# Kernel optimization log

Measured on AMD Instinct MI355X. Metric: run time of the kernel, lower is better.

Reference implementation:

```python
import jax, jax.numpy as jnp
import numpy as np
import math

B, L, DM = 8, 4096, 512            # batch, seq len (LQ == LK required by mean-fill quirk), model dim
DK, DV, C = 512, 512, 5            # projected dims, sampling factor
U_K = min(int(C * math.ceil(math.log(L))), L)  # 45 sampled keys
U_Q = min(int(C * math.ceil(math.log(L))), L)  # 45 top queries
SCALE = 1.0 / math.sqrt(DM)        # original divides by sqrt(d) where d = input dm


def setup_inputs() -> dict:
    key = jax.random.key(0)
    ks = jax.random.split(key, 10)
    w = 1.0 / math.sqrt(DM)
    # sample key indices per batch WITHOUT replacement (matches jax.random.choice(replace=False))
    kidx = jax.vmap(lambda k: jax.random.choice(k, L, shape=(U_K,), replace=False))(
        jax.random.split(ks[9], B)).astype(jnp.int32)
    return {
        "Q": jax.random.normal(ks[0], (B, L, DM), jnp.float32),
        "K": jax.random.normal(ks[1], (B, L, DM), jnp.float32),
        "V": jax.random.normal(ks[2], (B, L, DM), jnp.float32),
        "WQ": jax.random.normal(ks[3], (DM, DK), jnp.float32) * w,
        "bQ": jnp.zeros((DK,), jnp.float32),
        "WK": jax.random.normal(ks[4], (DM, DK), jnp.float32) * w,
        "bK": jnp.zeros((DK,), jnp.float32),
        "WV": jax.random.normal(ks[5], (DM, DV), jnp.float32) * w,
        "bV": jnp.zeros((DV,), jnp.float32),
        "kidx": kidx,
    }


def reference(Q, K, V, WQ, bQ, WK, bK, WV, bV, kidx):
    # dense projections (compute-dominant)
    Qp = Q @ WQ + bQ          # [B, L, DK]
    Kp = K @ WK + bK          # [B, L, DK]
    Vp = V @ WV + bV          # [B, L, DV]

    def per_sample(qp, kp, vp, idx):
        kbar = kp[idx]                                 # [U_K, DK] random key gather
        sbar = qp @ kbar.T                             # [L, U_K] sampled scores
        meas = jnp.max(sbar, axis=1) - jnp.mean(sbar, axis=1)  # sparsity measurement [L]
        _, I = jax.lax.top_k(meas, U_Q)                # top-u query indices
        qbar = qp[I]                                   # [U_Q, DK]
        attn = jax.nn.softmax(qbar @ kp.T * SCALE, axis=-1)    # [U_Q, L]
        s1 = attn @ vp                                 # [U_Q, DV]
        # faithful quirk: mean over FEATURE axis of V, broadcast to [L, DV]
        base = jnp.broadcast_to(jnp.mean(vp, axis=1, keepdims=True), (L, DV))
        return base.at[I].set(s1)                      # scatter selected rows

    return jax.vmap(per_sample)(Qp, Kp, Vp, kidx)      # [B, L, DV]
```

## Files before the change

kernel.cpp:

```cpp
#include <hip/hip_runtime.h>
#include <math.h>

static constexpr int B_ = 8;
static constexpr int L_ = 4096;
static constexpr int D_ = 512;
static constexpr int U_ = 45;
static constexpr float SCALE_ = 0.04419417382415922f;

static constexpr size_t OFF_WVMEAN = 0;
static constexpr size_t OFF_BV     = 512;
static constexpr size_t OFF_WQT    = 576;
static constexpr size_t OFF_WKT    = OFF_WQT + 262144;
static constexpr size_t OFF_KBAR   = OFF_WKT + 262144;
static constexpr size_t OFF_KW     = OFF_KBAR + 184320;
static constexpr size_t OFF_CVEC   = OFF_KW + 184320;
static constexpr size_t OFF_MEAS   = OFF_CVEC + 384;
static constexpr size_t OFF_TOPI   = OFF_MEAS + 32768;
static constexpr size_t OFF_QBAR   = OFF_TOPI + 384;
static constexpr size_t OFF_QW     = OFF_QBAR + 184320;
static constexpr size_t OFF_DVEC   = OFF_QW + 184320;
static constexpr size_t OFF_SC     = OFF_DVEC + 384;
static constexpr size_t OFF_PART   = OFF_SC + 1474560;
static constexpr size_t OFF_ATTNV  = OFF_PART + 1474560;
static constexpr size_t OFF_S1     = OFF_ATTNV + 184320;

__device__ __forceinline__ float wave_sum(float v) {
  #pragma unroll
  for (int m = 32; m; m >>= 1) v += __shfl_xor(v, m, 64);
  return v;
}
__device__ __forceinline__ float wave_max(float v) {
  #pragma unroll
  for (int m = 32; m; m >>= 1) v = fmaxf(v, __shfl_xor(v, m, 64));
  return v;
}

__global__ __launch_bounds__(256) void transpose_k(const float* __restrict__ WQ,
    const float* __restrict__ WK, float* __restrict__ wqt, float* __restrict__ wkt) {
  const float* src = blockIdx.z ? WK : WQ;
  float* dst = blockIdx.z ? wkt : wqt;
  __shared__ float tile[32][33];
  int tx = threadIdx.x, ty = threadIdx.y;
  int x = blockIdx.x * 32 + tx;
  int y0 = blockIdx.y * 32;
  for (int r = ty; r < 32; r += 8) tile[r][tx] = src[(size_t)(y0 + r) * 512 + x];
  __syncthreads();
  int xo = y0 + tx;
  int yo0 = blockIdx.x * 32;
  for (int r = ty; r < 32; r += 8) dst[(size_t)(yo0 + r) * 512 + xo] = tile[tx][r];
}

__global__ __launch_bounds__(256) void wvmean_k(const float* __restrict__ WV,
    const float* __restrict__ bV, float* __restrict__ wvmean, float* __restrict__ bvout) {
  int t = threadIdx.x, w = t >> 6, lane = t & 63;
  const float4* W4 = (const float4*)WV;
  int mbase = (blockIdx.x * 4 + w) * 16;
  for (int i = 0; i < 16; ++i) {
    int m = mbase + i;
    float4 a = W4[(size_t)m * 128 + lane];
    float4 c = W4[(size_t)m * 128 + 64 + lane];
    float s = ((a.x + a.y) + (a.z + a.w)) + ((c.x + c.y) + (c.z + c.w));
    s = wave_sum(s);
    if (lane == 0) wvmean[m] = s * (1.0f / 512.0f);
  }
  if (blockIdx.x == 0 && w == 0) {
    const float4* b4 = (const float4*)bV;
    float4 a = b4[lane], c = b4[64 + lane];
    float s = ((a.x + a.y) + (a.z + a.w)) + ((c.x + c.y) + (c.z + c.w));
    s = wave_sum(s);
    if (lane == 0) bvout[0] = s * (1.0f / 512.0f);
  }
}

__global__ __launch_bounds__(512) void rows_matmul_k(const float* __restrict__ src,
    const int* __restrict__ idx, const float* __restrict__ W, const float* __restrict__ bias,
    const float* __restrict__ avec, float* __restrict__ aux, float* __restrict__ out) {
  int blk = blockIdx.x;
  int b = blk / 9, g = blk % 9;
  int j0 = g * 5;
  int t = threadIdx.x;
  __shared__ float rows[5][512];
  for (int r = 0; r < 5; ++r) {
    int j = j0 + r;
    const float* s = idx ? (src + ((size_t)b * L_ + idx[b * U_ + j]) * 512)
                         : (src + ((size_t)(b * U_ + j)) * 512);
    rows[r][t] = s[t];
  }
  __syncthreads();
  float bi = bias ? bias[t] : 0.0f;
  float a0 = bi, a1 = bi, a2 = bi, a3 = bi, a4 = bi;
  #pragma unroll 4
  for (int m = 0; m < 512; ++m) {
    float wv = W[(size_t)m * 512 + t];
    a0 = fmaf(rows[0][m], wv, a0);
    a1 = fmaf(rows[1][m], wv, a1);
    a2 = fmaf(rows[2][m], wv, a2);
    a3 = fmaf(rows[3][m], wv, a3);
    a4 = fmaf(rows[4][m], wv, a4);
  }
  out[((size_t)(b * U_ + j0 + 0)) * 512 + t] = a0;
  out[((size_t)(b * U_ + j0 + 1)) * 512 + t] = a1;
  out[((size_t)(b * U_ + j0 + 2)) * 512 + t] = a2;
  out[((size_t)(b * U_ + j0 + 3)) * 512 + t] = a3;
  out[((size_t)(b * U_ + j0 + 4)) * 512 + t] = a4;
  if (avec) {
    float av = avec[t];
    __shared__ float red[8];
    float accs[5] = {a0, a1, a2, a3, a4};
    #pragma unroll
    for (int r = 0; r < 5; ++r) {
      float v = wave_sum(accs[r] * av);
      if ((t & 63) == 0) red[t >> 6] = v;
      __syncthreads();
      if (t == 0) {
        float s2 = 0.0f;
        #pragma unroll
        for (int k2 = 0; k2 < 8; ++k2) s2 += red[k2];
        aux[b * U_ + j0 + r] = s2;
      }
      __syncthreads();
    }
  }
}

__global__ __launch_bounds__(256) void meas2_k(const float* __restrict__ Q,
    const float* __restrict__ kw, const float* __restrict__ cvec, float* __restrict__ meas) {
  const int b = blockIdx.y;
  const int l0 = blockIdx.x * 64;
  const int t = threadIdx.x;
  const int tx = t & 15, ty = t >> 4;
  const int rswz = (ty >> 1) & 3;

  __shared__ float Qs[64][68];
  __shared__ float Ks[48][68];

  float acc[4][3];
  #pragma unroll
  for (int i = 0; i < 4; ++i) { acc[i][0] = 0.f; acc[i][1] = 0.f; acc[i][2] = 0.f; }

  const float4* Q4  = (const float4*)(Q + ((size_t)b * L_ + l0) * 512);
  const float4* kw4 = (const float4*)(kw + (size_t)b * U_ * 512);

  float4 pq[4], pk[3];
  int lr[4], lc[4], kr[3], kc[3];
  #pragma unroll
  for (int p = 0; p < 4; ++p) { int idx = p * 256 + t; lr[p] = idx >> 4; lc[p] = idx & 15; }
  #pragma unroll
  for (int p = 0; p < 3; ++p) { int idx = p * 256 + t; kr[p] = idx >> 4; kc[p] = idx & 15; }

  #pragma unroll
  for (int p = 0; p < 4; ++p) pq[p] = Q4[(size_t)lr[p] * 128 + lc[p]];
  #pragma unroll
  for (int p = 0; p < 3; ++p)
    pk[p] = (kr[p] < U_) ? kw4[(size_t)kr[p] * 128 + kc[p]] : make_float4(0.f, 0.f, 0.f, 0.f);

  #pragma unroll
  for (int p = 0; p < 4; ++p) {
    int sw = (lr[p] >> 3) & 3;
    *(float4*)&Qs[lr[p]][(lc[p] ^ sw) * 4] = pq[p];
  }
  #pragma unroll
  for (int p = 0; p < 3; ++p) *(float4*)&Ks[kr[p]][kc[p] * 4] = pk[p];
  __syncthreads();

  for (int it = 0; it < 8; ++it) {
    if (it < 7) {
      int k0 = (it + 1) * 16;
      #pragma unroll
      for (int p = 0; p < 4; ++p) pq[p] = Q4[(size_t)lr[p] * 128 + k0 + lc[p]];
      #pragma unroll
      for (int p = 0; p < 3; ++p)
        pk[p] = (kr[p] < U_) ? kw4[(size_t)kr[p] * 128 + k0 + kc[p]] : make_float4(0.f, 0.f, 0.f, 0.f);
    }
    #pragma unroll 4
    for (int kk4 = 0; kk4 < 16; ++kk4) {
      float4 kv0 = *(const float4*)&Ks[tx * 3 + 0][kk4 * 4];
      float4 kv1 = *(const float4*)&Ks[tx * 3 + 1][kk4 * 4];
      float4 kv2 = *(const float4*)&Ks[tx * 3 + 2][kk4 * 4];
      int qc = (kk4 ^ rswz) * 4;
      #pragma unroll
      for (int i = 0; i < 4; ++i) {
        float4 qv = *(const float4*)&Qs[ty * 4 + i][qc];
        acc[i][0] = fmaf(qv.x, kv0.x, acc[i][0]); acc[i][0] = fmaf(qv.y, kv0.y, acc[i][0]);
        acc[i][0] = fmaf(qv.z, kv0.z, acc[i][0]); acc[i][0] = fmaf(qv.w, kv0.w, acc[i][0]);
        acc[i][1] = fmaf(qv.x, kv1.x, acc[i][1]); acc[i][1] = fmaf(qv.y, kv1.y, acc[i][1]);
        acc[i][1] = fmaf(qv.z, kv1.z, acc[i][1]); acc[i][1] = fmaf(qv.w, kv1.w, acc[i][1]);
        acc[i][2] = fmaf(qv.x, kv2.x, acc[i][2]); acc[i][2] = fmaf(qv.y, kv2.y, acc[i][2]);
        acc[i][2] = fmaf(qv.z, kv2.z, acc[i][2]); acc[i][2] = fmaf(qv.w, kv2.w, acc[i][2]);
      }
    }
    __syncthreads();
    if (it < 7) {
      #pragma unroll
      for (int p = 0; p < 4; ++p) {
        int sw = (lr[p] >> 3) & 3;
        *(float4*)&Qs[lr[p]][(lc[p] ^ sw) * 4] = pq[p];
      }
      #pragma unroll
      for (int p = 0; p < 3; ++p) *(float4*)&Ks[kr[p]][kc[p] * 4] = pk[p];
      __syncthreads();
    }
  }

  const bool valid = (tx < 15);
  float c0 = 0.f, c1 = 0.f, c2 = 0.f;
  if (valid) {
    c0 = cvec[b * U_ + tx * 3 + 0];
    c1 = cvec[b * U_ + tx * 3 + 1];
    c2 = cvec[b * U_ + tx * 3 + 2];
  }
  #pragma unroll
  for (int i = 0; i < 4; ++i) {
    float s0 = acc[i][0] + c0, s1 = acc[i][1] + c1, s2 = acc[i][2] + c2;
    float jmax = valid ? fmaxf(fmaxf(s0, s1), s2) : -3.4e38f;
    float jsum = valid ? (s0 + s1 + s2) : 0.f;
    #pragma unroll
    for (int m = 8; m; m >>= 1) {
      jmax = fmaxf(jmax, __shfl_xor(jmax, m, 64));
      jsum += __shfl_xor(jsum, m, 64);
    }
    if (tx == 0) meas[(size_t)b * L_ + l0 + ty * 4 + i] = jmax - jsum * (1.0f / 45.0f);
  }
}

__global__ __launch_bounds__(256) void scores2_k(const float* __restrict__ K,
    const float* __restrict__ qw, const float* __restrict__ dvec, float* __restrict__ sc) {
  const int b = blockIdx.y;
  const int l0 = blockIdx.x * 64;
  const int t = threadIdx.x;
  const int tx = t & 15, ty = t >> 4;
  const int rswz = (ty >> 1) & 3;

  __shared__ float Qs[64][68];
  __shared__ float Ks[48][68];

  float acc[4][3];
  #pragma unroll
  for (int i = 0; i < 4; ++i) { acc[i][0] = 0.f; acc[i][1] = 0.f; acc[i][2] = 0.f; }

  const float4* K4  = (const float4*)(K + ((size_t)b * L_ + l0) * 512);
  const float4* qw4 = (const float4*)(qw + (size_t)b * U_ * 512);

  float4 pq[4], pk[3];
  int lr[4], lc[4], kr[3], kc[3];
  #pragma unroll
  for (int p = 0; p < 4; ++p) { int idx = p * 256 + t; lr[p] = idx >> 4; lc[p] = idx & 15; }
  #pragma unroll
  for (int p = 0; p < 3; ++p) { int idx = p * 256 + t; kr[p] = idx >> 4; kc[p] = idx & 15; }

  #pragma unroll
  for (int p = 0; p < 4; ++p) pq[p] = K4[(size_t)lr[p] * 128 + lc[p]];
  #pragma unroll
  for (int p = 0; p < 3; ++p)
    pk[p] = (kr[p] < U_) ? qw4[(size_t)kr[p] * 128 + kc[p]] : make_float4(0.f, 0.f, 0.f, 0.f);

  #pragma unroll
  for (int p = 0; p < 4; ++p) {
    int sw = (lr[p] >> 3) & 3;
    *(float4*)&Qs[lr[p]][(lc[p] ^ sw) * 4] = pq[p];
  }
  #pragma unroll
  for (int p = 0; p < 3; ++p) *(float4*)&Ks[kr[p]][kc[p] * 4] = pk[p];
  __syncthreads();

  for (int it = 0; it < 8; ++it) {
    if (it < 7) {
      int k0 = (it + 1) * 16;
      #pragma unroll
      for (int p = 0; p < 4; ++p) pq[p] = K4[(size_t)lr[p] * 128 + k0 + lc[p]];
      #pragma unroll
      for (int p = 0; p < 3; ++p)
        pk[p] = (kr[p] < U_) ? qw4[(size_t)kr[p] * 128 + k0 + kc[p]] : make_float4(0.f, 0.f, 0.f, 0.f);
    }
    #pragma unroll 4
    for (int kk4 = 0; kk4 < 16; ++kk4) {
      float4 kv0 = *(const float4*)&Ks[tx * 3 + 0][kk4 * 4];
      float4 kv1 = *(const float4*)&Ks[tx * 3 + 1][kk4 * 4];
      float4 kv2 = *(const float4*)&Ks[tx * 3 + 2][kk4 * 4];
      int qc = (kk4 ^ rswz) * 4;
      #pragma unroll
      for (int i = 0; i < 4; ++i) {
        float4 qv = *(const float4*)&Qs[ty * 4 + i][qc];
        acc[i][0] = fmaf(qv.x, kv0.x, acc[i][0]); acc[i][0] = fmaf(qv.y, kv0.y, acc[i][0]);
        acc[i][0] = fmaf(qv.z, kv0.z, acc[i][0]); acc[i][0] = fmaf(qv.w, kv0.w, acc[i][0]);
        acc[i][1] = fmaf(qv.x, kv1.x, acc[i][1]); acc[i][1] = fmaf(qv.y, kv1.y, acc[i][1]);
        acc[i][1] = fmaf(qv.z, kv1.z, acc[i][1]); acc[i][1] = fmaf(qv.w, kv1.w, acc[i][1]);
        acc[i][2] = fmaf(qv.x, kv2.x, acc[i][2]); acc[i][2] = fmaf(qv.y, kv2.y, acc[i][2]);
        acc[i][2] = fmaf(qv.z, kv2.z, acc[i][2]); acc[i][2] = fmaf(qv.w, kv2.w, acc[i][2]);
      }
    }
    __syncthreads();
    if (it < 7) {
      #pragma unroll
      for (int p = 0; p < 4; ++p) {
        int sw = (lr[p] >> 3) & 3;
        *(float4*)&Qs[lr[p]][(lc[p] ^ sw) * 4] = pq[p];
      }
      #pragma unroll
      for (int p = 0; p < 3; ++p) *(float4*)&Ks[kr[p]][kc[p] * 4] = pk[p];
      __syncthreads();
    }
  }

  if (tx < 15) {
    float d0 = dvec[b * U_ + tx * 3 + 0];
    float d1 = dvec[b * U_ + tx * 3 + 1];
    float d2 = dvec[b * U_ + tx * 3 + 2];
    #pragma unroll
    for (int i = 0; i < 4; ++i) {
      int l = l0 + ty * 4 + i;
      sc[((size_t)(b * U_ + tx * 3 + 0)) * 4096 + l] = (acc[i][0] + d0) * SCALE_;
      sc[((size_t)(b * U_ + tx * 3 + 1)) * 4096 + l] = (acc[i][1] + d1) * SCALE_;
      sc[((size_t)(b * U_ + tx * 3 + 2)) * 4096 + l] = (acc[i][2] + d2) * SCALE_;
    }
  }
}

__global__ __launch_bounds__(256) void topk_k(const float* __restrict__ meas, int* __restrict__ topI) {
  int b = blockIdx.x, t = threadIdx.x;
  __shared__ unsigned long long keys[4096];
  __shared__ unsigned long long wred[4];
  for (int i = t; i < 4096; i += 256) {
    float m = meas[(size_t)b * 4096 + i];
    unsigned u = __float_as_uint(m);
    u = (u & 0x80000000u) ? ~u : (u | 0x80000000u);
    keys[i] = ((unsigned long long)u << 32) | (unsigned)(4095 - i);
  }
  __syncthreads();
  for (int it = 0; it < U_; ++it) {
    unsigned long long lm = 0ull;
    for (int i = t; i < 4096; i += 256) { unsigned long long k = keys[i]; lm = k > lm ? k : lm; }
    #pragma unroll
    for (int m = 32; m; m >>= 1) { unsigned long long o = __shfl_xor(lm, m, 64); lm = o > lm ? o : lm; }
    if ((t & 63) == 0) wred[t >> 6] = lm;
    __syncthreads();
    if (t == 0) {
      unsigned long long f = wred[0];
      for (int k2 = 1; k2 < 4; ++k2) f = wred[k2] > f ? wred[k2] : f;
      int idxl = 4095 - (int)(f & 0xFFFFFFFFull);
      topI[b * U_ + it] = idxl;
      keys[idxl] = 0ull;
    }
    __syncthreads();
  }
}

__global__ __launch_bounds__(256) void softmax_k(float* __restrict__ sc) {
  int row = blockIdx.x;
  int t = threadIdx.x;
  float* s = sc + (size_t)row * 4096;
  __shared__ float buf[4096];
  __shared__ float red[4];
  float4* b4 = (float4*)buf;
  float4* s4 = (float4*)s;
  float lmax = -3.4e38f;
  for (int i = t; i < 1024; i += 256) {
    float4 v = s4[i]; b4[i] = v;
    lmax = fmaxf(lmax, fmaxf(fmaxf(v.x, v.y), fmaxf(v.z, v.w)));
  }
  lmax = wave_max(lmax);
  if ((t & 63) == 0) red[t >> 6] = lmax;
  __syncthreads();
  float mx = fmaxf(fmaxf(red[0], red[1]), fmaxf(red[2], red[3]));
  __syncthreads();
  float lsum = 0.0f;
  for (int i = t; i < 1024; i += 256) {
    float4 v = b4[i];
    v.x = expf(v.x - mx); v.y = expf(v.y - mx); v.z = expf(v.z - mx); v.w = expf(v.w - mx);
    b4[i] = v;
    lsum += (v.x + v.y) + (v.z + v.w);
  }
  lsum = wave_sum(lsum);
  if ((t & 63) == 0) red[t >> 6] = lsum;
  __syncthreads();
  float inv = 1.0f / (red[0] + red[1] + red[2] + red[3]);
  for (int i = t; i < 1024; i += 256) {
    float4 v = b4[i];
    v.x *= inv; v.y *= inv; v.z *= inv; v.w *= inv;
    s4[i] = v;
  }
}

__global__ __launch_bounds__(256) void attnv5_k(const float* __restrict__ V,
    const float* __restrict__ attn, float* __restrict__ part) {
  const int b = blockIdx.x, ks = blockIdx.y, dh = blockIdx.z;
  const int d0 = dh * 64;
  const int t = threadIdx.x;
  const int tx = t & 15, ty = t >> 4;

  __shared__ float As[2][48][68];
  __shared__ float Vs[2][64][68];

  const float* attnb = attn + (size_t)b * U_ * 4096 + (size_t)ks * 512;
  const float* Vb = V + ((size_t)b * L_ + (size_t)ks * 512) * 512 + d0;

  const int vrow = t >> 4, vc4 = t & 15;
  int arow[3], ac4[3], arr[3];
  #pragma unroll
  for (int p = 0; p < 3; ++p) {
    int idx = p * 256 + t;
    arow[p] = idx >> 4; ac4[p] = idx & 15;
    arr[p] = arow[p] < U_ ? arow[p] : U_ - 1;
  }

  float4 pv0, pv1, pv2, pv3, pa0, pa1, pa2;

#define ISSUE(S) do { const int lb_ = (S) * 64;                                  \
    pv0 = *(const float4*)&Vb[(size_t)(lb_ + vrow +  0) * 512 + vc4 * 4];        \
    pv1 = *(const float4*)&Vb[(size_t)(lb_ + vrow + 16) * 512 + vc4 * 4];        \
    pv2 = *(const float4*)&Vb[(size_t)(lb_ + vrow + 32) * 512 + vc4 * 4];        \
    pv3 = *(const float4*)&Vb[(size_t)(lb_ + vrow + 48) * 512 + vc4 * 4];        \
    pa0 = *(const float4*)&attnb[(size_t)arr[0] * 4096 + lb_ + ac4[0] * 4];      \
    pa1 = *(const float4*)&attnb[(size_t)arr[1] * 4096 + lb_ + ac4[1] * 4];      \
    pa2 = *(const float4*)&attnb[(size_t)arr[2] * 4096 + lb_ + ac4[2] * 4];      \
  } while (0)

#define COMMIT(BUF) do {                                                         \
    *(float4*)&Vs[BUF][vrow +  0][vc4 * 4] = pv0;                                \
    *(float4*)&Vs[BUF][vrow + 16][vc4 * 4] = pv1;                                \
    *(float4*)&Vs[BUF][vrow + 32][vc4 * 4] = pv2;                                \
    *(float4*)&Vs[BUF][vrow + 48][vc4 * 4] = pv3;                                \
    *(float4*)&As[BUF][arow[0]][ac4[0] * 4] = pa0;                               \
    *(float4*)&As[BUF][arow[1]][ac4[1] * 4] = pa1;                               \
    *(float4*)&As[BUF][arow[2]][ac4[2] * 4] = pa2;                               \
  } while (0)

  float4 acc0 = make_float4(0.f, 0.f, 0.f, 0.f);
  float4 acc1 = make_float4(0.f, 0.f, 0.f, 0.f);
  float4 acc2 = make_float4(0.f, 0.f, 0.f, 0.f);

  ISSUE(0);
  asm volatile("s_waitcnt vmcnt(0)" ::: "memory");
  COMMIT(0);
  ISSUE(1);
  asm volatile("s_waitcnt lgkmcnt(0)" ::: "memory");
  __builtin_amdgcn_s_barrier();
  __builtin_amdgcn_sched_barrier(0);

  #pragma unroll 1
  for (int s = 0; s < 8; ++s) {
    const int rb = s & 1;
    #pragma unroll 4
    for (int l4 = 0; l4 < 16; ++l4) {
      float4 q0 = *(const float4*)&As[rb][tx * 3 + 0][l4 * 4];
      float4 q1 = *(const float4*)&As[rb][tx * 3 + 1][l4 * 4];
      float4 q2 = *(const float4*)&As[rb][tx * 3 + 2][l4 * 4];
      #pragma unroll
      for (int j = 0; j < 4; ++j) {
        float4 v = *(const float4*)&Vs[rb][l4 * 4 + j][ty * 4];
        float a0 = (j == 0) ? q0.x : (j == 1) ? q0.y : (j == 2) ? q0.z : q0.w;
        float a1 = (j == 0) ? q1.x : (j == 1) ? q1.y : (j == 2) ? q1.z : q1.w;
        float a2 = (j == 0) ? q2.x : (j == 1) ? q2.y : (j == 2) ? q2.z : q2.w;
        acc0.x = fmaf(a0, v.x, acc0.x); acc0.y = fmaf(a0, v.y, acc0.y);
        acc0.z = fmaf(a0, v.z, acc0.z); acc0.w = fmaf(a0, v.w, acc0.w);
        acc1.x = fmaf(a1, v.x, acc1.x); acc1.y = fmaf(a1, v.y, acc1.y);
        acc1.z = fmaf(a1, v.z, acc1.z); acc1.w = fmaf(a1, v.w, acc1.w);
        acc2.x = fmaf(a2, v.x, acc2.x); acc2.y = fmaf(a2, v.y, acc2.y);
        acc2.z = fmaf(a2, v.z, acc2.z); acc2.w = fmaf(a2, v.w, acc2.w);
      }
    }
    if (s + 1 < 8) {
      asm volatile("s_waitcnt vmcnt(0)" ::: "memory");
      COMMIT((s + 1) & 1);
      if (s + 2 < 8) ISSUE(s + 2);
      asm volatile("s_waitcnt lgkmcnt(0)" ::: "memory");
      __builtin_amdgcn_s_barrier();
      __builtin_amdgcn_sched_barrier(0);
    }
  }
#undef ISSUE
#undef COMMIT

  {
    float* dstbase = part + (((size_t)(ks * 8 + b)) * U_) * 512 + d0 + ty * 4;
    int i0 = tx * 3;
    if (i0 + 0 < U_) *(float4*)(dstbase + (size_t)(i0 + 0) * 512) = acc0;
    if (i0 + 1 < U_) *(float4*)(dstbase + (size_t)(i0 + 1) * 512) = acc1;
    if (i0 + 2 < U_) *(float4*)(dstbase + (size_t)(i0 + 2) * 512) = acc2;
  }
}

__global__ __launch_bounds__(256) void attnvred_k(const float* __restrict__ part,
                                                  float* __restrict__ av) {
  int x = blockIdx.x * 256 + threadIdx.x;
  float s = 0.0f;
  #pragma unroll
  for (int ls = 0; ls < 8; ++ls) s += part[(size_t)ls * 184320 + x];
  av[x] = s;
}

__global__ __launch_bounds__(256) void output_k(const float* __restrict__ V,
    const float* __restrict__ wvmean, const float* __restrict__ bvp,
    const int* __restrict__ topI, const float* __restrict__ s1, float* __restrict__ outp) {
  int b = blockIdx.y, tile = blockIdx.x;
  int l0 = tile * 64;
  int t = threadIdx.x, w = t >> 6, lane = t & 63;
  __shared__ int sel[64];
  if (t < 64) sel[t] = -1;
  __syncthreads();
  if (t < U_) {
    int lj = topI[b * U_ + t] - l0;
    if (lj >= 0 && lj < 64) sel[lj] = t;
  }
  __syncthreads();
  const float4* wv4 = (const float4*)wvmean;
  float4 wa = wv4[lane], wb = wv4[64 + lane];
  float bv = bvp[0];
  const float4* V4 = (const float4*)(V + (size_t)b * L_ * 512);
  float4* out4 = (float4*)(outp + (size_t)b * L_ * 512);
  const float4* s14 = (const float4*)s1;
  for (int r = w; r < 64; r += 4) {
    int l = l0 + r;
    int j = sel[r];
    float4 o1, o2;
    if (j >= 0) {
      o1 = s14[((size_t)(b * U_ + j)) * 128 + lane];
      o2 = s14[((size_t)(b * U_ + j)) * 128 + 64 + lane];
    } else {
      float4 va = V4[(size_t)l * 128 + lane];
      float4 vb = V4[(size_t)l * 128 + 64 + lane];
      float s = va.x * wa.x + va.y * wa.y + va.z * wa.z + va.w * wa.w
              + vb.x * wb.x + vb.y * wb.y + vb.z * wb.z + vb.w * wb.w;
      s = wave_sum(s);
      float base = s + bv;
      o1 = make_float4(base, base, base, base);
      o2 = o1;
    }
    out4[(size_t)l * 128 + lane] = o1;
    out4[(size_t)l * 128 + 64 + lane] = o2;
  }
}

extern "C" void kernel_launch(void* const* d_in, const int* in_sizes, int n_in,
                              void* d_out, int out_size, void* d_ws, size_t ws_size,
                              hipStream_t stream) {
  (void)in_sizes; (void)n_in; (void)out_size; (void)ws_size;
  const float* Q  = (const float*)d_in[0];
  const float* K  = (const float*)d_in[1];
  const float* V  = (const float*)d_in[2];
  const float* WQ = (const float*)d_in[3];
  const float* bQ = (const float*)d_in[4];
  const float* WK = (const float*)d_in[5];
  const float* bK = (const float*)d_in[6];
  const float* WV = (const float*)d_in[7];
  const float* bV = (const float*)d_in[8];
  const int* kidx = (const int*)d_in[9];
  float* ws = (float*)d_ws;
  float* out = (float*)d_out;

  float* wvmean = ws + OFF_WVMEAN;
  float* bvm    = ws + OFF_BV;
  float* wqt    = ws + OFF_WQT;
  float* wkt    = ws + OFF_WKT;
  float* kbar   = ws + OFF_KBAR;
  float* kw     = ws + OFF_KW;
  float* cvec   = ws + OFF_CVEC;
  float* measp  = ws + OFF_MEAS;
  int*   topI   = (int*)(ws + OFF_TOPI);
  float* qbar   = ws + OFF_QBAR;
  float* qw     = ws + OFF_QW;
  float* dvec   = ws + OFF_DVEC;
  float* sc     = ws + OFF_SC;
  float* partp  = ws + OFF_PART;
  float* attnv  = ws + OFF_ATTNV;
  float* s1     = ws + OFF_S1;

  transpose_k<<<dim3(16, 16, 2), dim3(32, 8), 0, stream>>>(WQ, WK, wqt, wkt);
  wvmean_k<<<dim3(8), dim3(256), 0, stream>>>(WV, bV, wvmean, bvm);

  rows_matmul_k<<<dim3(72), dim3(512), 0, stream>>>(K, kidx, WK, bK, bQ, cvec, kbar);
  rows_matmul_k<<<dim3(72), dim3(512), 0, stream>>>(kbar, nullptr, wqt, nullptr, nullptr, nullptr, kw);
  meas2_k<<<dim3(64, 8), dim3(256), 0, stream>>>(Q, kw, cvec, measp);
  topk_k<<<dim3(8), dim3(256), 0, stream>>>(measp, topI);
  rows_matmul_k<<<dim3(72), dim3(512), 0, stream>>>(Q, topI, WQ, bQ, bK, dvec, qbar);
  rows_matmul_k<<<dim3(72), dim3(512), 0, stream>>>(qbar, nullptr, wkt, nullptr, nullptr, nullptr, qw);
  scores2_k<<<dim3(64, 8), dim3(256), 0, stream>>>(K, qw, dvec, sc);
  softmax_k<<<dim3(360), dim3(256), 0, stream>>>(sc);
  attnv5_k<<<dim3(8, 8, 8), dim3(256), 0, stream>>>(V, sc, partp);
  attnvred_k<<<dim3(720), dim3(256), 0, stream>>>(partp, attnv);
  rows_matmul_k<<<dim3(72), dim3(512), 0, stream>>>(attnv, nullptr, WV, bV, nullptr, nullptr, s1);
  output_k<<<dim3(64, 8), dim3(256), 0, stream>>>(V, wvmean, bvm, topI, s1, out);
}
```

Baseline: 447.3 us.

## Double-buffer LDS and enlarge tiles in sampled-score GEMM kernels

Replaces the meas2/scores2 kernels with a shared macro-based kernel that tiles 128 rows per block with 6 key columns per thread, and double-buffers the Q/K tiles in LDS. It issues the global loads two stages ahead and uses explicit waitcnt/s_barrier, so each k-step needs one barrier instead of two. Out-of-range key rows are clamped rather than zero-filled, and those columns are masked at the end. The aim is to overlap global loads with FMA work and raise arithmetic intensity per LDS read. The cost is more LDS and registers, and only half as many blocks (256), which may lower occupancy.

```diff
diff --git a/kernel.cpp b/kernel.cpp
--- a/kernel.cpp
+++ b/kernel.cpp
@@ -123,198 +123,145 @@
   }
 }
 
-__global__ __launch_bounds__(256) void meas2_k(const float* __restrict__ Q,
+
+#define M3_DECLS                                                               \
+  const int t = threadIdx.x;                                                   \
+  const int tx = t & 7, ty = t >> 3;                                           \
+  const int qsw = ty & 3;                                                      \
+  __shared__ float Qs[2][128][68];                                             \
+  __shared__ float Ks[2][48][68];                                              \
+  int lr[8], lc[8], kr[3], kc[3], krr[3];                                      \
+  _Pragma("unroll") for (int p = 0; p < 8; ++p) {                              \
+    int idx = p * 256 + t; lr[p] = idx >> 4; lc[p] = idx & 15; }               \
+  _Pragma("unroll") for (int p = 0; p < 3; ++p) {                              \
+    int idx = p * 256 + t; kr[p] = idx >> 4; kc[p] = idx & 15;                 \
+    krr[p] = kr[p] < U_ ? kr[p] : U_ - 1; }                                    \
+  float4 pq[8], pk[3];                                                         \
+  float acc[4][6];                                                             \
+  _Pragma("unroll") for (int i = 0; i < 4; ++i)                                \
+    _Pragma("unroll") for (int r = 0; r < 6; ++r) acc[i][r] = 0.f;
+
+#define M3_ISSUE(S) do { const int k0_ = (S) * 16;                             \
+    _Pragma("unroll") for (int p = 0; p < 8; ++p)                              \
+      pq[p] = X4[(size_t)lr[p] * 128 + k0_ + lc[p]];                           \
+    _Pragma("unroll") for (int p = 0; p < 3; ++p)                              \
+      pk[p] = W4[(size_t)krr[p] * 128 + k0_ + kc[p]];                          \
+  } while (0)
+
+#define M3_COMMIT(B) do {                                                      \
+    _Pragma("unroll") for (int p = 0; p < 8; ++p)                              \
+      *(float4*)&Qs[B][lr[p]][(lc[p] ^ ((lr[p] >> 2) & 3)) * 4] = pq[p];       \
+    _Pragma("unroll") for (int p = 0; p < 3; ++p)                              \
+      *(float4*)&Ks[B][kr[p]][kc[p] * 4] = pk[p];                              \
+  } while (0)
+
+#define M3_PIPELINE                                                            \
+  M3_ISSUE(0);                                                                 \
+  asm volatile("s_waitcnt vmcnt(0)" ::: "memory");                             \
+  M3_COMMIT(0);                                                                \
+  M3_ISSUE(1);                                                                 \
+  asm volatile("s_waitcnt lgkmcnt(0)" ::: "memory");                           \
+  __builtin_amdgcn_s_barrier();                                                \
+  __builtin_amdgcn_sched_barrier(0);                                           \
+  _Pragma("unroll 1")                                                          \
+  for (int s = 0; s < 8; ++s) {                                                \
+    const int rb = s & 1;                                                      \
+    _Pragma("unroll 4")                                                        \
+    for (int kk4 = 0; kk4 < 16; ++kk4) {                                       \
+      float4 kv0 = *(const float4*)&Ks[rb][tx * 6 + 0][kk4 * 4];               \
+      float4 kv1 = *(const float4*)&Ks[rb][tx * 6 + 1][kk4 * 4];               \
+      float4 kv2 = *(const float4*)&Ks[rb][tx * 6 + 2][kk4 * 4];               \
+      float4 kv3 = *(const float4*)&Ks[rb][tx * 6 + 3][kk4 * 4];               \
+      float4 kv4 = *(const float4*)&Ks[rb][tx * 6 + 4][kk4 * 4];               \
+      float4 kv5 = *(const float4*)&Ks[rb][tx * 6 + 5][kk4 * 4];               \
+      const int qc = (kk4 ^ qsw) * 4;                                          \
+      _Pragma("unroll") for (int i = 0; i < 4; ++i) {                          \
+        float4 qv = *(const float4*)&Qs[rb][ty * 4 + i][qc];                   \
+        acc[i][0] = fmaf(qv.x, kv0.x, acc[i][0]); acc[i][0] = fmaf(qv.y, kv0.y, acc[i][0]); \
+        acc[i][0] = fmaf(qv.z, kv0.z, acc[i][0]); acc[i][0] = fmaf(qv.w, kv0.w, acc[i][0]); \
+        acc[i][1] = fmaf(qv.x, kv1.x, acc[i][1]); acc[i][1] = fmaf(qv.y, kv1.y, acc[i][1]); \
+        acc[i][1] = fmaf(qv.z, kv1.z, acc[i][1]); acc[i][1] = fmaf(qv.w, kv1.w, acc[i][1]); \
+        acc[i][2] = fmaf(qv.x, kv2.x, acc[i][2]); acc[i][2] = fmaf(qv.y, kv2.y, acc[i][2]); \
+        acc[i][2] = fmaf(qv.z, kv2.z, acc[i][2]); acc[i][2] = fmaf(qv.w, kv2.w, acc[i][2]); \
+        acc[i][3] = fmaf(qv.x, kv3.x, acc[i][3]); acc[i][3] = fmaf(qv.y, kv3.y, acc[i][3]); \
+        acc[i][3] = fmaf(qv.z, kv3.z, acc[i][3]); acc[i][3] = fmaf(qv.w, kv3.w, acc[i][3]); \
+        acc[i][4] = fmaf(qv.x, kv4.x, acc[i][4]); acc[i][4] = fmaf(qv.y, kv4.y, acc[i][4]); \
+        acc[i][4] = fmaf(qv.z, kv4.z, acc[i][4]); acc[i][4] = fmaf(qv.w, kv4.w, acc[i][4]); \
+        acc[i][5] = fmaf(qv.x, kv5.x, acc[i][5]); acc[i][5] = fmaf(qv.y, kv5.y, acc[i][5]); \
+        acc[i][5] = fmaf(qv.z, kv5.z, acc[i][5]); acc[i][5] = fmaf(qv.w, kv5.w, acc[i][5]); \
+      }                                                                        \
+    }                                                                          \
+    if (s + 1 < 8) {                                                           \
+      asm volatile("s_waitcnt vmcnt(0)" ::: "memory");                         \
+      M3_COMMIT((s + 1) & 1);                                                  \
+      if (s + 2 < 8) M3_ISSUE(s + 2);                                          \
+      asm volatile("s_waitcnt lgkmcnt(0)" ::: "memory");                       \
+      __builtin_amdgcn_s_barrier();                                            \
+      __builtin_amdgcn_sched_barrier(0);                                       \
+    }                                                                          \
+  }
+
+__global__ __launch_bounds__(256) void meas3_k(const float* __restrict__ Q,
     const float* __restrict__ kw, const float* __restrict__ cvec, float* __restrict__ meas) {
   const int b = blockIdx.y;
-  const int l0 = blockIdx.x * 64;
-  const int t = threadIdx.x;
-  const int tx = t & 15, ty = t >> 4;
-  const int rswz = (ty >> 1) & 3;
-
-  __shared__ float Qs[64][68];
-  __shared__ float Ks[48][68];
-
-  float acc[4][3];
-  #pragma unroll
-  for (int i = 0; i < 4; ++i) { acc[i][0] = 0.f; acc[i][1] = 0.f; acc[i][2] = 0.f; }
-
-  const float4* Q4  = (const float4*)(Q + ((size_t)b * L_ + l0) * 512);
-  const float4* kw4 = (const float4*)(kw + (size_t)b * U_ * 512);
-
-  float4 pq[4], pk[3];
-  int lr[4], lc[4], kr[3], kc[3];
-  #pragma unroll
-  for (int p = 0; p < 4; ++p) { int idx = p * 256 + t; lr[p] = idx >> 4; lc[p] = idx & 15; }
-  #pragma unroll
-  for (int p = 0; p < 3; ++p) { int idx = p * 256 + t; kr[p] = idx >> 4; kc[p] = idx & 15; }
-
-  #pragma unroll
-  for (int p = 0; p < 4; ++p) pq[p] = Q4[(size_t)lr[p] * 128 + lc[p]];
-  #pragma unroll
-  for (int p = 0; p < 3; ++p)
-    pk[p] = (kr[p] < U_) ? kw4[(size_t)kr[p] * 128 + kc[p]] : make_float4(0.f, 0.f, 0.f, 0.f);
-
-  #pragma unroll
-  for (int p = 0; p < 4; ++p) {
-    int sw = (lr[p] >> 3) & 3;
-    *(float4*)&Qs[lr[p]][(lc[p] ^ sw) * 4] = pq[p];
-  }
-  #pragma unroll
-  for (int p = 0; p < 3; ++p) *(float4*)&Ks[kr[p]][kc[p] * 4] = pk[p];
-  __syncthreads();
-
-  for (int it = 0; it < 8; ++it) {
-    if (it < 7) {
-      int k0 = (it + 1) * 16;
-      #pragma unroll
-      for (int p = 0; p < 4; ++p) pq[p] = Q4[(size_t)lr[p] * 128 + k0 + lc[p]];
-      #pragma unroll
-      for (int p = 0; p < 3; ++p)
-        pk[p] = (kr[p] < U_) ? kw4[(size_t)kr[p] * 128 + k0 + kc[p]] : make_float4(0.f, 0.f, 0.f, 0.f);
-    }
-    #pragma unroll 4
-    for (int kk4 = 0; kk4 < 16; ++kk4) {
-      float4 kv0 = *(const float4*)&Ks[tx * 3 + 0][kk4 * 4];
-      float4 kv1 = *(const float4*)&Ks[tx * 3 + 1][kk4 * 4];
-      float4 kv2 = *(const float4*)&Ks[tx * 3 + 2][kk4 * 4];
-      int qc = (kk4 ^ rswz) * 4;
-      #pragma unroll
-      for (int i = 0; i < 4; ++i) {
-        float4 qv = *(const float4*)&Qs[ty * 4 + i][qc];
-        acc[i][0] = fmaf(qv.x, kv0.x, acc[i][0]); acc[i][0] = fmaf(qv.y, kv0.y, acc[i][0]);
-        acc[i][0] = fmaf(qv.z, kv0.z, acc[i][0]); acc[i][0] = fmaf(qv.w, kv0.w, acc[i][0]);
-        acc[i][1] = fmaf(qv.x, kv1.x, acc[i][1]); acc[i][1] = fmaf(qv.y, kv1.y, acc[i][1]);
-        acc[i][1] = fmaf(qv.z, kv1.z, acc[i][1]); acc[i][1] = fmaf(qv.w, kv1.w, acc[i][1]);
-        acc[i][2] = fmaf(qv.x, kv2.x, acc[i][2]); acc[i][2] = fmaf(qv.y, kv2.y, acc[i][2]);
-        acc[i][2] = fmaf(qv.z, kv2.z, acc[i][2]); acc[i][2] = fmaf(qv.w, kv2.w, acc[i][2]);
+  const int l0 = blockIdx.x * 128;
+  const float4* X4 = (const float4*)(Q + ((size_t)b * L_ + l0) * 512);
+  const float4* W4 = (const float4*)(kw + (size_t)b * U_ * 512);
+  M3_DECLS
+  M3_PIPELINE
+
+  float cj[6]; bool vj[6];
+  #pragma unroll
+  for (int r = 0; r < 6; ++r) {
+    int j = tx * 6 + r;
+    vj[r] = (j < U_);
+    cj[r] = vj[r] ? cvec[b * U_ + j] : 0.f;
+  }
+  #pragma unroll
+  for (int i = 0; i < 4; ++i) {
+    float rmax = -3.4e38f, rsum = 0.f;
+    #pragma unroll
+    for (int r = 0; r < 6; ++r) {
+      if (vj[r]) {
+        float s = acc[i][r] + cj[r];
+        rmax = fmaxf(rmax, s);
+        rsum += s;
       }
     }
-    __syncthreads();
-    if (it < 7) {
-      #pragma unroll
-      for (int p = 0; p < 4; ++p) {
-        int sw = (lr[p] >> 3) & 3;
-        *(float4*)&Qs[lr[p]][(lc[p] ^ sw) * 4] = pq[p];
-      }
-      #pragma unroll
-      for (int p = 0; p < 3; ++p) *(float4*)&Ks[kr[p]][kc[p] * 4] = pk[p];
-      __syncthreads();
-    }
-  }
-
-  const bool valid = (tx < 15);
-  float c0 = 0.f, c1 = 0.f, c2 = 0.f;
-  if (valid) {
-    c0 = cvec[b * U_ + tx * 3 + 0];
-    c1 = cvec[b * U_ + tx * 3 + 1];
-    c2 = cvec[b * U_ + tx * 3 + 2];
-  }
-  #pragma unroll
-  for (int i = 0; i < 4; ++i) {
-    float s0 = acc[i][0] + c0, s1 = acc[i][1] + c1, s2 = acc[i][2] + c2;
-    float jmax = valid ? fmaxf(fmaxf(s0, s1), s2) : -3.4e38f;
-    float jsum = valid ? (s0 + s1 + s2) : 0.f;
     #pragma unroll
-    for (int m = 8; m; m >>= 1) {
-      jmax = fmaxf(jmax, __shfl_xor(jmax, m, 64));
-      jsum += __shfl_xor(jsum, m, 64);
-    }
-    if (tx == 0) meas[(size_t)b * L_ + l0 + ty * 4 + i] = jmax - jsum * (1.0f / 45.0f);
-  }
-}
-
-__global__ __launch_bounds__(256) void scores2_k(const float* __restrict__ K,
+    for (int m = 4; m; m >>= 1) {
+      rmax = fmaxf(rmax, __shfl_xor(rmax, m, 64));
+      rsum += __shfl_xor(rsum, m, 64);
+    }
+    if (tx == 0) meas[(size_t)b * L_ + l0 + ty * 4 + i] = rmax - rsum * (1.0f / 45.0f);
+  }
+}
+
+__global__ __launch_bounds__(256) void scores3_k(const float* __restrict__ K,
     const float* __restrict__ qw, const float* __restrict__ dvec, float* __restrict__ sc) {
   const int b = blockIdx.y;
-  const int l0 = blockIdx.x * 64;
-  const int t = threadIdx.x;
-  const int tx = t & 15, ty = t >> 4;
-  const int rswz = (ty >> 1) & 3;
-
-  __shared__ float Qs[64][68];
-  __shared__ float Ks[48][68];
-
-  float acc[4][3];
-  #pragma unroll
-  for (int i = 0; i < 4; ++i) { acc[i][0] = 0.f; acc[i][1] = 0.f; acc[i][2] = 0.f; }
-
-  const float4* K4  = (const float4*)(K + ((size_t)b * L_ + l0) * 512);
-  const float4* qw4 = (const float4*)(qw + (size_t)b * U_ * 512);
-
-  float4 pq[4], pk[3];
-  int lr[4], lc[4], kr[3], kc[3];
-  #pragma unroll
-  for (int p = 0; p < 4; ++p) { int idx = p * 256 + t; lr[p] = idx >> 4; lc[p] = idx & 15; }
-  #pragma unroll
-  for (int p = 0; p < 3; ++p) { int idx = p * 256 + t; kr[p] = idx >> 4; kc[p] = idx & 15; }
-
-  #pragma unroll
-  for (int p = 0; p < 4; ++p) pq[p] = K4[(size_t)lr[p] * 128 + lc[p]];
-  #pragma unroll
-  for (int p = 0; p < 3; ++p)
-    pk[p] = (kr[p] < U_) ? qw4[(size_t)kr[p] * 128 + kc[p]] : make_float4(0.f, 0.f, 0.f, 0.f);
-
-  #pragma unroll
-  for (int p = 0; p < 4; ++p) {
-    int sw = (lr[p] >> 3) & 3;
-    *(float4*)&Qs[lr[p]][(lc[p] ^ sw) * 4] = pq[p];
-  }
-  #pragma unroll
-  for (int p = 0; p < 3; ++p) *(float4*)&Ks[kr[p]][kc[p] * 4] = pk[p];
-  __syncthreads();
-
-  for (int it = 0; it < 8; ++it) {
-    if (it < 7) {
-      int k0 = (it + 1) * 16;
+  const int l0 = blockIdx.x * 128;
+  const float4* X4 = (const float4*)(K + ((size_t)b * L_ + l0) * 512);
+  const float4* W4 = (const float4*)(qw + (size_t)b * U_ * 512);
+  M3_DECLS
+  M3_PIPELINE
+
+  #pragma unroll
+  for (int r = 0; r < 6; ++r) {
+    int j = tx * 6 + r;
+    if (j < U_) {
+      float dj = dvec[b * U_ + j];
+      float* dst = sc + ((size_t)(b * U_ + j)) * 4096 + l0 + ty * 4;
       #pragma unroll
-      for (int p = 0; p < 4; ++p) pq[p] = K4[(size_t)lr[p] * 128 + k0 + lc[p]];
-      #pragma unroll
-      for (int p = 0; p < 3; ++p)
-        pk[p] = (kr[p] < U_) ? qw4[(size_t)kr[p] * 128 + k0 + kc[p]] : make_float4(0.f, 0.f, 0.f, 0.f);
-    }
-    #pragma unroll 4
-    for (int kk4 = 0; kk4 < 16; ++kk4) {
-      float4 kv0 = *(const float4*)&Ks[tx * 3 + 0][kk4 * 4];
-      float4 kv1 = *(const float4*)&Ks[tx * 3 + 1][kk4 * 4];
-      float4 kv2 = *(const float4*)&Ks[tx * 3 + 2][kk4 * 4];
-      int qc = (kk4 ^ rswz) * 4;
-      #pragma unroll
-      for (int i = 0; i < 4; ++i) {
-        float4 qv = *(const float4*)&Qs[ty * 4 + i][qc];
-        acc[i][0] = fmaf(qv.x, kv0.x, acc[i][0]); acc[i][0] = fmaf(qv.y, kv0.y, acc[i][0]);
-        acc[i][0] = fmaf(qv.z, kv0.z, acc[i][0]); acc[i][0] = fmaf(qv.w, kv0.w, acc[i][0]);
-        acc[i][1] = fmaf(qv.x, kv1.x, acc[i][1]); acc[i][1] = fmaf(qv.y, kv1.y, acc[i][1]);
-        acc[i][1] = fmaf(qv.z, kv1.z, acc[i][1]); acc[i][1] = fmaf(qv.w, kv1.w, acc[i][1]);
-        acc[i][2] = fmaf(qv.x, kv2.x, acc[i][2]); acc[i][2] = fmaf(qv.y, kv2.y, acc[i][2]);
-        acc[i][2] = fmaf(qv.z, kv2.z, acc[i][2]); acc[i][2] = fmaf(qv.w, kv2.w, acc[i][2]);
-      }
-    }
-    __syncthreads();
-    if (it < 7) {
-      #pragma unroll
-      for (int p = 0; p < 4; ++p) {
-        int sw = (lr[p] >> 3) & 3;
-        *(float4*)&Qs[lr[p]][(lc[p] ^ sw) * 4] = pq[p];
-      }
-      #pragma unroll
-      for (int p = 0; p < 3; ++p) *(float4*)&Ks[kr[p]][kc[p] * 4] = pk[p];
-      __syncthreads();
-    }
-  }
-
-  if (tx < 15) {
-    float d0 = dvec[b * U_ + tx * 3 + 0];
-    float d1 = dvec[b * U_ + tx * 3 + 1];
-    float d2 = dvec[b * U_ + tx * 3 + 2];
-    #pragma unroll
-    for (int i = 0; i < 4; ++i) {
-      int l = l0 + ty * 4 + i;
-      sc[((size_t)(b * U_ + tx * 3 + 0)) * 4096 + l] = (acc[i][0] + d0) * SCALE_;
-      sc[((size_t)(b * U_ + tx * 3 + 1)) * 4096 + l] = (acc[i][1] + d1) * SCALE_;
-      sc[((size_t)(b * U_ + tx * 3 + 2)) * 4096 + l] = (acc[i][2] + d2) * SCALE_;
-    }
-  }
-}
+      for (int i = 0; i < 4; ++i) dst[i] = (acc[i][r] + dj) * SCALE_;
+    }
+  }
+}
+
+#undef M3_DECLS
+#undef M3_ISSUE
+#undef M3_COMMIT
+#undef M3_PIPELINE
 
 __global__ __launch_bounds__(256) void topk_k(const float* __restrict__ meas, int* __restrict__ topI) {
   int b = blockIdx.x, t = threadIdx.x;
@@ -570,11 +517,11 @@
 
   rows_matmul_k<<<dim3(72), dim3(512), 0, stream>>>(K, kidx, WK, bK, bQ, cvec, kbar);
   rows_matmul_k<<<dim3(72), dim3(512), 0, stream>>>(kbar, nullptr, wqt, nullptr, nullptr, nullptr, kw);
-  meas2_k<<<dim3(64, 8), dim3(256), 0, stream>>>(Q, kw, cvec, measp);
+  meas3_k<<<dim3(32, 8), dim3(256), 0, stream>>>(Q, kw, cvec, measp);
   topk_k<<<dim3(8), dim3(256), 0, stream>>>(measp, topI);
   rows_matmul_k<<<dim3(72), dim3(512), 0, stream>>>(Q, topI, WQ, bQ, bK, dvec, qbar);
   rows_matmul_k<<<dim3(72), dim3(512), 0, stream>>>(qbar, nullptr, wkt, nullptr, nullptr, nullptr, qw);
-  scores2_k<<<dim3(64, 8), dim3(256), 0, stream>>>(K, qw, dvec, sc);
+  scores3_k<<<dim3(32, 8), dim3(256), 0, stream>>>(K, qw, dvec, sc);
   softmax_k<<<dim3(360), dim3(256), 0, stream>>>(sc);
   attnv5_k<<<dim3(8, 8, 8), dim3(256), 0, stream>>>(V, sc, partp);
   attnvred_k<<<dim3(720), dim3(256), 0, stream>>>(partp, attnv);
```

After: 486.8 us. +8.8%, slower.
